# Kernel optimization log

Measured on AMD Instinct MI355X. Metric: run time of the kernel, lower is better.

Reference implementation:

```python
import jax, jax.numpy as jnp
import numpy as np

N = 4096          # total ensemble boxes per frame
M = 20            # MAX_MERGE_NUMS
H = 16            # MergeNet hidden_c
COND_THRES = 0.2
IOU_THRES = 0.3


def setup_inputs() -> dict:
    key = jax.random.key(0)
    ks = jax.random.split(key, 6)
    u = jax.random.uniform(ks[0], (N, 9), dtype=jnp.float32)
    # realistic lidar boxes: centers in a ~140x80x8m range, dims in [0.5, 4.5), heading in [-pi, pi)
    centers = (u[:, 0:3] - 0.5) * jnp.array([140.0, 80.0, 8.0], jnp.float32)
    dims = u[:, 3:6] * 4.0 + 0.5
    heading = (u[:, 6:7] - 0.5) * (2.0 * np.pi)
    extra = u[:, 7:9]  # extra box attrs (cols 7:9), untouched by merge
    pred_boxes = jnp.concatenate([centers, dims, heading, extra], axis=-1)
    pred_scores = jax.random.uniform(ks[1], (N,), dtype=jnp.float32)
    pred_labels = jax.random.randint(ks[2], (N,), 0, 3)
    w1 = (jax.random.normal(ks[3], (M, H), jnp.float32) / np.sqrt(M)).astype(jnp.float32)
    b1 = jnp.zeros((H,), jnp.float32)
    w2 = (jax.random.normal(ks[4], (H, H), jnp.float32) / np.sqrt(H)).astype(jnp.float32)
    b2 = jnp.zeros((H,), jnp.float32)
    w3 = (jax.random.normal(ks[5], (H, 1), jnp.float32) / np.sqrt(H)).astype(jnp.float32)
    b3 = jnp.zeros((1,), jnp.float32)
    return dict(pred_boxes=pred_boxes, pred_scores=pred_scores, pred_labels=pred_labels,
                w1=w1, b1=b1, w2=w2, b2=b2, w3=w3, b3=b3)


def _bev_aligned(b):
    # boxes3d_lidar_to_aligned_bev_boxes: swap dx/dy when |limit_period(heading)| >= pi/4
    ang = b[..., 6] - jnp.floor(b[..., 6] / np.pi + 0.5) * np.pi
    swap = jnp.abs(ang) >= (np.pi / 4)
    dx = jnp.where(swap, b[..., 4], b[..., 3])
    dy = jnp.where(swap, b[..., 3], b[..., 4])
    return jnp.stack([b[..., 0] - dx / 2, b[..., 1] - dy / 2,
                      b[..., 0] + dx / 2, b[..., 1] + dy / 2], axis=-1)


def _iou_one_many(a, b):
    # axis-aligned BEV IoU of one box a[4] vs many b[N,4]
    xmin = jnp.maximum(a[0], b[:, 0]); ymin = jnp.maximum(a[1], b[:, 1])
    xmax = jnp.minimum(a[2], b[:, 2]); ymax = jnp.minimum(a[3], b[:, 3])
    inter = jnp.maximum(xmax - xmin, 0.0) * jnp.maximum(ymax - ymin, 0.0)
    area_a = (a[2] - a[0]) * (a[3] - a[1])
    area_b = (b[:, 2] - b[:, 0]) * (b[:, 3] - b[:, 1])
    return inter / jnp.maximum(area_a + area_b - inter, 1e-6)


def _nms_merge(pred_boxes, pred_scores, pred_labels, w1, b1, w2, b2, w3, b3):
    valid = pred_scores > COND_THRES
    sort_key = jnp.where(valid, pred_scores, -jnp.inf)
    order = jnp.argsort(-sort_key)                 # descending by score; invalid sink
    boxes9 = pred_boxes[order]
    labels = pred_labels[order]
    scores = pred_scores[order]
    suppressed0 = ~valid[order]
    boxes7 = boxes9[:, :7]
    bev0 = _bev_aligned(boxes7)                    # merged boxes get suppressed, so bev is static

    def mergenet(ob):                              # ob: [M, 7] -> merged box [7]
        x = ob.T                                   # [7, M] (k is the feature axis)
        h = jax.nn.relu(x @ w1 + b1)
        h = jax.nn.relu(h @ w2 + b2)
        return (h @ w3 + b3)[:, 0]

    def step(suppressed, i):
        active = ~suppressed[i]
        same = (labels == labels[i]) & (~suppressed)
        iou = _iou_one_many(bev0[i], bev0)         # [N]
        over = (iou > IOU_THRES) & same            # includes self (iou=1)
        count = jnp.sum(over)
        rank = jnp.cumsum(over) - 1                # slot of each overlap, in score order
        tgt = jnp.where(over & (rank < M), rank, M)
        ob = jnp.zeros((M, 7), boxes7.dtype).at[tgt].set(boxes7, mode='drop')
        bi = boxes7[i]
        new_box = jnp.where(count > 1, mergenet(ob), bi)
        new_box = new_box.at[3:6].set(jnp.maximum(new_box[3:6], 1e-5))
        out_box = jnp.where(active, new_box, bi)
        return suppressed | (over & active), (out_box, active)

    _, (merged7, keep) = jax.lax.scan(step, suppressed0, jnp.arange(N))
    out_boxes = jnp.concatenate([merged7, boxes9[:, 7:9]], axis=-1)   # [N, 9]
    return out_boxes, scores, labels, keep


def reference(pred_boxes, pred_scores, pred_labels, w1, b1, w2, b2, w3, b3):
    # Returns fixed-shape (boxes9, scores, labels, keep_mask); rows with keep=False
    # correspond to boxes that torch's dynamic version would have removed.
    return _nms_merge(pred_boxes, pred_scores, pred_labels, w1, b1, w2, b2, w3, b3)
```

## Files before the change

### kernel.cpp

```cpp
#include <hip/hip_runtime.h>
#include <cstdint>

typedef unsigned long long u64;
typedef unsigned int u32;

#define NB 4096
#define NW 64
#define MM 20
#define HH 16
#define COND_THRES 0.2f
#define IOU_THRES 0.3f
#define PI_F  3.14159265358979323846f
#define PI4_F 0.78539816339744830962f

#define NTILE 2080

#define WS_MASK    32768
#define WS_BOX9S   (WS_MASK + NB*NW*8)
#define WS_BEVS    (WS_BOX9S + NB*9*4)
#define WS_SCORES  (WS_BEVS + NB*16)
#define WS_LABELS  (WS_SCORES + NB*4)
#define WS_NBRW    (WS_LABELS + NB*4)
#define WS_SUPSTEP (WS_NBRW + NB*8)
#define WS_CNT     (WS_SUPSTEP + NB*4)
#define WS_SLOTW   (WS_CNT + NB*4)
#define WS_SLOTI   (WS_SLOTW + NB*16)
#define WS_CSARR   (WS_SLOTI + NB*8)

__device__ __forceinline__ u64 sort_key(float s, int i) {
  u32 sb = (s > COND_THRES) ? __float_as_uint(s) : 0u;
  return ((u64)(sb ^ 0xFFFFFFFFu) << 12) | (u64)i;
}

__global__ void __launch_bounds__(256) k_prep(const float* __restrict__ scores,
                                              const float* __restrict__ boxes9,
                                              const int* __restrict__ labels,
                                              float* __restrict__ box9s, float4* __restrict__ bevs,
                                              float* __restrict__ scoress, int* __restrict__ labelss,
                                              u64* __restrict__ nbrw, u32* __restrict__ cnt) {
  #pragma clang fp contract(off)
  __shared__ u64 keys[NB];
  __shared__ u32 part[16][16];
  int tid = threadIdx.x;
  for (int k = tid; k < NB; k += 256) keys[k] = sort_key(scores[k], k);
  __syncthreads();
  int bl = tid & 15;
  int ch = tid >> 4;
  u64 ki = keys[blockIdx.x * 16 + bl];
  int c = 0;
  #pragma unroll 16
  for (int t = 0; t < 256; ++t) c += (keys[(ch << 8) + t] < ki) ? 1 : 0;
  part[bl][ch] = (u32)c;
  __syncthreads();
  if (tid < 16) {
    int i = blockIdx.x * 16 + tid;
    int r = 0;
    #pragma unroll
    for (int q = 0; q < 16; ++q) r += (int)part[tid][q];
    nbrw[i] = 0;
    cnt[i] = 0;
    float b[9];
    #pragma unroll
    for (int f = 0; f < 9; ++f) b[f] = boxes9[i * 9 + f];
    #pragma unroll
    for (int f = 0; f < 9; ++f) box9s[r * 9 + f] = b[f];
    float ang = b[6] - floorf(b[6] / PI_F + 0.5f) * PI_F;
    bool sw = fabsf(ang) >= PI4_F;
    float dx = sw ? b[4] : b[3];
    float dy = sw ? b[3] : b[4];
    bevs[r] = make_float4(b[0] - dx * 0.5f, b[1] - dy * 0.5f,
                          b[0] + dx * 0.5f, b[1] + dy * 0.5f);
    scoress[r] = scores[i];
    labelss[r] = labels[i];
  }
}

__global__ void __launch_bounds__(64) k_mask(const float4* __restrict__ bevs,
                                             const int* __restrict__ labelss,
                                             const float* __restrict__ scoress,
                                             u64* __restrict__ mask,
                                             u64* __restrict__ nbrw,
                                             u32* __restrict__ cnt,
                                             u64* __restrict__ slotW,
                                             u32* __restrict__ slotI,
                                             u64* __restrict__ csArr) {
  #pragma clang fp contract(off)
  __shared__ float4 bj[64];
  __shared__ int lj[64];
  __shared__ u64 tw[64];
  int t = threadIdx.x;
  int b = blockIdx.x;
  int it = (int)((sqrtf(8.0f * (float)b + 1.0f) - 1.0f) * 0.5f);
  while ((it + 1) * (it + 2) / 2 <= b) ++it;
  while (it * (it + 1) / 2 > b) --it;
  int jt = b - it * (it + 1) / 2;
  int j = jt * 64 + t;
  bj[t] = bevs[j];
  lj[t] = labelss[j];
  u64 vj = __ballot(scoress[j] > COND_THRES);
  int i = it * 64 + t;
  float4 a = bevs[i];
  int la = labelss[i];
  float area_a = (a.z - a.x) * (a.w - a.y);
  __syncthreads();
  u64 w = 0;
  #pragma unroll 8
  for (int kk = 0; kk < 64; ++kk) {
    float4 bb = bj[kk];
    float xmin = fmaxf(a.x, bb.x), ymin = fmaxf(a.y, bb.y);
    float xmax = fminf(a.z, bb.z), ymax = fminf(a.w, bb.w);
    float inter = fmaxf(xmax - xmin, 0.0f) * fmaxf(ymax - ymin, 0.0f);
    float area_b = (bb.z - bb.x) * (bb.w - bb.y);
    float iou = inter / fmaxf(area_a + area_b - inter, 1e-6f);
    if ((iou > IOU_THRES) && (la == lj[kk])) w |= (1ull << kk);
  }
  mask[(u64)i * NW + jt] = w;
  if (jt == it) {
    csArr[i] = w & ((1ull << t) - 1ull);
  } else {
    if (w & vj) {
      u32 pos = atomicAdd(&cnt[i], 1u);
      if (pos < 2u) { slotW[i * 2 + pos] = w; slotI[i * 2 + pos] = (u32)jt; }
      atomicOr(&nbrw[i], 1ull << jt);
    }
  }
  if (jt < it) {
    tw[t] = w;
    __syncthreads();
    u64 wT = 0;
    #pragma unroll 8
    for (int k = 0; k < 64; ++k) wT |= ((tw[k] >> t) & 1ull) << k;
    mask[(u64)j * NW + it] = wT;
  }
}

__global__ void __launch_bounds__(1024) k_nms(const u64* __restrict__ mask,
                                              const u64* __restrict__ nbrw,
                                              const u32* __restrict__ cnt,
                                              const u64* __restrict__ slotW,
                                              const u32* __restrict__ slotI,
                                              const u64* __restrict__ csArr,
                                              const float* __restrict__ scoress,
                                              int* __restrict__ supstep) {
  __shared__ u64 csL[NB];
  __shared__ u64 c0L[NB];
  __shared__ u64 c1L[NB];
  __shared__ u64 remL[NB];
  __shared__ u32 i01L[NB];
  __shared__ u64 vwL[64];
  __shared__ u64 keptL[64];
  int tid = threadIdx.x;
  int lane = tid & 63;
  int waveId = tid >> 6;
  #pragma unroll
  for (int s4 = 0; s4 < 4; ++s4) {
    int i = tid + (s4 << 10);
    bool v = scoress[i] > COND_THRES;
    u64 vb = __ballot(v);
    if (lane == 0) vwL[waveId + (s4 << 4)] = vb;
  }
  #pragma unroll
  for (int s4 = 0; s4 < 4; ++s4) {
    int i = tid + (s4 << 10);
    u32 c = cnt[i];
    u64 c0 = 0, c1 = 0; u32 i0 = 0, i1 = 0;
    if (c >= 1u) { c0 = slotW[i * 2];     i0 = slotI[i * 2]; }
    if (c >= 2u) { c1 = slotW[i * 2 + 1]; i1 = slotI[i * 2 + 1]; }
    u32 n = c > 2u ? 2u : c;
    u32 ovf = c > 2u ? 1u : 0u;
    u64 rem = 0;
    if (ovf) rem = nbrw[i] & ~(1ull << i0) & ~(1ull << i1);
    csL[i] = csArr[i];
    c0L[i] = c0; c1L[i] = c1; remL[i] = rem;
    i01L[i] = i0 | (i1 << 6) | (n << 12) | (ovf << 14);
  }
  __syncthreads();
  if (tid < 64) {
    u64 keptW = 0;
    u64 cs_c = csL[lane], c0_c = c0L[lane], c1_c = c1L[lane], rem_c = remL[lane];
    u32 m_c = i01L[lane];
    u64 vws_c = vwL[0];
    for (int s = 0; s < 64; ++s) {
      u64 cs_n = 0, c0_n = 0, c1_n = 0, rem_n = 0, vws_n = 0; u32 m_n = 0;
      if (s < 63) {
        int ip = ((s + 1) << 6) | lane;
        cs_n = csL[ip]; c0_n = c0L[ip]; c1_n = c1L[ip];
        rem_n = remL[ip]; m_n = i01L[ip]; vws_n = vwL[s + 1];
      }
      int w0 = (int)(m_c & 63u), w1 = (int)((m_c >> 6) & 63u);
      u64 k0 = __shfl(keptW, w0);
      u64 k1 = __shfl(keptW, w1);
      bool hk = ((c0_c & k0) | (c1_c & k1)) != 0ull;
      u64 rem = rem_c;
      while (__ballot(rem != 0ull) != 0ull) {
        int w = rem ? __builtin_ctzll(rem) : 0;
        u64 kws = __shfl(keptW, w);
        if (rem) {
          u64 m = mask[(u64)((s << 6) | lane) * NW + w];
          hk = hk || ((m & kws) != 0ull);
          rem &= rem - 1;
        }
      }
      u64 dw = ~vws_c;
      u64 kw = 0;
      bool und = (vws_c >> lane) & 1ull;
      while (true) {
        bool dec = und && ((cs_c & ~dw) == 0ull);
        bool keep = dec && !hk && ((cs_c & kw) == 0ull);
        dw |= __ballot(dec);
        kw |= __ballot(keep);
        und = und && !dec;
        if (__ballot(und) == 0ull) break;
      }
      if (lane == s) keptW = kw;
      cs_c = cs_n; c0_c = c0_n; c1_c = c1_n; rem_c = rem_n; m_c = m_n; vws_c = vws_n;
    }
    keptL[lane] = keptW;
  }
  __syncthreads();
  #pragma unroll
  for (int s4 = 0; s4 < 4; ++s4) {
    int j = tid + (s4 << 10);
    int wj = j >> 6;
    bool valid = (vwL[wj] >> (j & 63)) & 1ull;
    int res;
    if (!valid) {
      res = -1;
    } else {
      res = j;
      u32 m = i01L[j];
      u64 cs = csL[j];
      int cand = 0x7FFFFFFF;
      if (!(m & (1u << 14))) {
        u32 n = (m >> 12) & 3;
        if (n >= 1) {
          int w0 = (int)(m & 63u);
          u64 h = c0L[j] & keptL[w0];
          if (h) { int r = (w0 << 6) + __builtin_ctzll(h); if (r < cand) cand = r; }
        }
        if (n >= 2) {
          int w1 = (int)((m >> 6) & 63u);
          u64 h = c1L[j] & keptL[w1];
          if (h) { int r = (w1 << 6) + __builtin_ctzll(h); if (r < cand) cand = r; }
        }
        { u64 h = cs & keptL[wj];
          if (h) { int r = (wj << 6) + __builtin_ctzll(h); if (r < cand) cand = r; } }
      } else {
        u64 t = nbrw[j];
        while (t) {
          int w = __builtin_ctzll(t);
          t &= t - 1;
          u64 h = mask[(u64)j * NW + w] & keptL[w];
          if (h) { cand = (w << 6) + __builtin_ctzll(h); break; }
        }
        if (cand == 0x7FFFFFFF) {
          u64 h = cs & keptL[wj];
          if (h) cand = (wj << 6) + __builtin_ctzll(h);
        }
      }
      if (cand != 0x7FFFFFFF) res = cand;
    }
    supstep[j] = res;
  }
}

__global__ void __launch_bounds__(64) k_merge(
    const u64* __restrict__ mask, const int* __restrict__ supstep,
    const float* __restrict__ box9s, const float* __restrict__ scoress,
    const int* __restrict__ labelss,
    const float* __restrict__ w1, const float* __restrict__ b1,
    const float* __restrict__ w2, const float* __restrict__ b2,
    const float* __restrict__ w3, const float* __restrict__ b3,
    float* __restrict__ out) {
  #pragma clang fp contract(off)
  __shared__ int candList[MM];
  __shared__ float ob[MM][7];
  __shared__ float h1[7][HH];
  __shared__ float h2[7][HH];
  __shared__ float res[7];
  int i = blockIdx.x;
  int t = threadIdx.x;
  bool active = (supstep[i] == i);
  u64 wq = 0;
  int cnt = 0;
  if (active) {
    u64 w = mask[(u64)i * NW + t];
    while (w) {
      int b = __builtin_ctzll(w);
      w &= w - 1;
      int j = (t << 6) | b;
      if (supstep[j] >= i) { wq |= (1ull << b); cnt++; }
    }
  }
  int incl = cnt;
  #pragma unroll
  for (int off = 1; off < 64; off <<= 1) {
    int v = __shfl_up(incl, off);
    if (t >= off) incl += v;
  }
  int excl = incl - cnt;
  int count = __shfl(incl, 63);
  bool merged = active && (count > 1);
  if (merged && wq) {
    int pos = excl;
    u64 ww = wq;
    while (ww && pos < MM) {
      int b = __builtin_ctzll(ww);
      ww &= ww - 1;
      candList[pos++] = (t << 6) | b;
    }
  }
  __syncthreads();
  if (merged) {
    int nc = count < MM ? count : MM;
    if (t < MM) {
      if (t < nc) {
        int j = candList[t];
        #pragma unroll
        for (int f = 0; f < 7; ++f) ob[t][f] = box9s[j * 9 + f];
      } else {
        #pragma unroll
        for (int f = 0; f < 7; ++f) ob[t][f] = 0.0f;
      }
    }
    __syncthreads();
    for (int o = t; o < 7 * HH; o += 64) {
      int f = o >> 4, hh = o & 15;
      float acc = b1[hh];
      #pragma unroll
      for (int m = 0; m < MM; ++m) acc += ob[m][f] * w1[m * HH + hh];
      h1[f][hh] = fmaxf(acc, 0.0f);
    }
    __syncthreads();
    for (int o = t; o < 7 * HH; o += 64) {
      int f = o >> 4, oo = o & 15;
      float acc = b2[oo];
      #pragma unroll
      for (int k = 0; k < HH; ++k) acc += h1[f][k] * w2[k * HH + oo];
      h2[f][oo] = fmaxf(acc, 0.0f);
    }
    __syncthreads();
    if (t < 7) {
      float acc = b3[0];
      #pragma unroll
      for (int k = 0; k < HH; ++k) acc += h2[t][k] * w3[k];
      if (t >= 3 && t < 6) acc = fmaxf(acc, 1e-5f);
      res[t] = acc;
    }
    __syncthreads();
  }
  if (t < 9) {
    float v = box9s[i * 9 + t];
    if (merged && t < 7) v = res[t];
    out[i * 9 + t] = v;
  }
  if (t == 0) {
    out[NB * 9 + i]          = scoress[i];
    out[NB * 9 + NB + i]     = (float)labelss[i];
    out[NB * 9 + 2 * NB + i] = active ? 1.0f : 0.0f;
  }
}

extern "C" void kernel_launch(void* const* d_in, const int* in_sizes, int n_in,
                              void* d_out, int out_size, void* d_ws, size_t ws_size,
                              hipStream_t stream) {
  const float* boxes9 = (const float*)d_in[0];
  const float* scores = (const float*)d_in[1];
  const int*   labels = (const int*)d_in[2];
  const float* w1 = (const float*)d_in[3];
  const float* b1 = (const float*)d_in[4];
  const float* w2 = (const float*)d_in[5];
  const float* b2 = (const float*)d_in[6];
  const float* w3 = (const float*)d_in[7];
  const float* b3 = (const float*)d_in[8];
  char* ws = (char*)d_ws;
  u64*    mask    = (u64*)(ws + WS_MASK);
  float*  box9s   = (float*)(ws + WS_BOX9S);
  float4* bevs    = (float4*)(ws + WS_BEVS);
  float*  scoress = (float*)(ws + WS_SCORES);
  int*    labelss = (int*)(ws + WS_LABELS);
  u64*    nbrw    = (u64*)(ws + WS_NBRW);
  int*    supstep = (int*)(ws + WS_SUPSTEP);
  u32*    cnt     = (u32*)(ws + WS_CNT);
  u64*    slotW   = (u64*)(ws + WS_SLOTW);
  u32*    slotI   = (u32*)(ws + WS_SLOTI);
  u64*    csArr   = (u64*)(ws + WS_CSARR);
  float*  out     = (float*)d_out;

  hipLaunchKernelGGL(k_prep,  dim3(256),   dim3(256),  0, stream,
                     scores, boxes9, labels, box9s, bevs, scoress, labelss, nbrw, cnt);
  hipLaunchKernelGGL(k_mask,  dim3(NTILE), dim3(64),   0, stream,
                     bevs, labelss, scoress, mask, nbrw, cnt, slotW, slotI, csArr);
  hipLaunchKernelGGL(k_nms,   dim3(1),     dim3(1024), 0, stream,
                     mask, nbrw, cnt, slotW, slotI, csArr, scoress, supstep);
  hipLaunchKernelGGL(k_merge, dim3(NB),    dim3(64),   0, stream,
                     mask, supstep, box9s, scoress, labelss,
                     w1, b1, w2, b2, w3, b3, out);
}
```

Baseline: 125.4 us.

## Prefetch overflow mask words into a shared-memory pool for serial NMS scan

```diff
diff --git a/kernel.cpp b/kernel.cpp
--- a/kernel.cpp
+++ b/kernel.cpp
@@ -14,6 +14,7 @@
 #define PI4_F 0.78539816339744830962f
 
 #define NTILE 2080
+#define POOLP 3072
 
 #define WS_MASK    32768
 #define WS_BOX9S   (WS_MASK + NB*NW*8)
@@ -145,13 +146,17 @@
   __shared__ u64 csL[NB];
   __shared__ u64 c0L[NB];
   __shared__ u64 c1L[NB];
-  __shared__ u64 remL[NB];
-  __shared__ u32 i01L[NB];
+  __shared__ unsigned short i01L[NB];
+  __shared__ u32 povL[NB];
+  __shared__ u64 poolW[POOLP];
+  __shared__ unsigned char poolIdx[POOLP];
   __shared__ u64 vwL[64];
   __shared__ u64 keptL[64];
+  __shared__ u32 poolCnt;
   int tid = threadIdx.x;
   int lane = tid & 63;
   int waveId = tid >> 6;
+  if (tid == 0) poolCnt = 0;
   #pragma unroll
   for (int s4 = 0; s4 < 4; ++s4) {
     int i = tid + (s4 << 10);
@@ -159,6 +164,7 @@
     u64 vb = __ballot(v);
     if (lane == 0) vwL[waveId + (s4 << 4)] = vb;
   }
+  __syncthreads();
   #pragma unroll
   for (int s4 = 0; s4 < 4; ++s4) {
     int i = tid + (s4 << 10);
@@ -168,37 +174,62 @@
     if (c >= 2u) { c1 = slotW[i * 2 + 1]; i1 = slotI[i * 2 + 1]; }
     u32 n = c > 2u ? 2u : c;
     u32 ovf = c > 2u ? 1u : 0u;
-    u64 rem = 0;
-    if (ovf) rem = nbrw[i] & ~(1ull << i0) & ~(1ull << i1);
+    u32 pov = 0;
+    if (ovf) {
+      u64 t = nbrw[i] & ~(1ull << i0) & ~(1ull << i1);
+      u32 len = (u32)__popcll(t);
+      u32 off = atomicAdd(&poolCnt, len);
+      if (off + len <= (u32)POOLP) {
+        u32 k = 0;
+        while (t) {
+          int w = __builtin_ctzll(t);
+          t &= t - 1;
+          poolW[off + k] = mask[(u64)i * NW + w];
+          poolIdx[off + k] = (unsigned char)w;
+          ++k;
+        }
+        pov = off | (len << 16);
+      } else {
+        pov = 0x80000000u;
+      }
+    }
     csL[i] = csArr[i];
-    c0L[i] = c0; c1L[i] = c1; remL[i] = rem;
-    i01L[i] = i0 | (i1 << 6) | (n << 12) | (ovf << 14);
+    c0L[i] = c0; c1L[i] = c1;
+    i01L[i] = (unsigned short)(i0 | (i1 << 6) | (n << 12) | (ovf << 14));
+    povL[i] = pov;
   }
   __syncthreads();
   if (tid < 64) {
     u64 keptW = 0;
-    u64 cs_c = csL[lane], c0_c = c0L[lane], c1_c = c1L[lane], rem_c = remL[lane];
-    u32 m_c = i01L[lane];
+    u64 cs_c = csL[lane], c0_c = c0L[lane], c1_c = c1L[lane];
+    u32 m_c = i01L[lane], p_c = povL[lane];
     u64 vws_c = vwL[0];
     for (int s = 0; s < 64; ++s) {
-      u64 cs_n = 0, c0_n = 0, c1_n = 0, rem_n = 0, vws_n = 0; u32 m_n = 0;
+      u64 cs_n = 0, c0_n = 0, c1_n = 0, vws_n = 0; u32 m_n = 0, p_n = 0;
       if (s < 63) {
         int ip = ((s + 1) << 6) | lane;
         cs_n = csL[ip]; c0_n = c0L[ip]; c1_n = c1L[ip];
-        rem_n = remL[ip]; m_n = i01L[ip]; vws_n = vwL[s + 1];
+        m_n = i01L[ip]; p_n = povL[ip]; vws_n = vwL[s + 1];
       }
       int w0 = (int)(m_c & 63u), w1 = (int)((m_c >> 6) & 63u);
       u64 k0 = __shfl(keptW, w0);
       u64 k1 = __shfl(keptW, w1);
       bool hk = ((c0_c & k0) | (c1_c & k1)) != 0ull;
-      u64 rem = rem_c;
-      while (__ballot(rem != 0ull) != 0ull) {
-        int w = rem ? __builtin_ctzll(rem) : 0;
-        u64 kws = __shfl(keptW, w);
-        if (rem) {
-          u64 m = mask[(u64)((s << 6) | lane) * NW + w];
-          hk = hk || ((m & kws) != 0ull);
-          rem &= rem - 1;
+      if (m_c & (1u << 14)) {
+        if (!(p_c & 0x80000000u)) {
+          u32 off = p_c & 0xFFFFu, len = (p_c >> 16) & 0xFFu;
+          for (u32 k = 0; k < len; ++k) {
+            int w = poolIdx[off + k];
+            hk = hk || ((poolW[off + k] & keptL[w]) != 0ull);
+          }
+        } else {
+          int i = (s << 6) | lane;
+          u64 t = nbrw[i];
+          while (t) {
+            int w = __builtin_ctzll(t);
+            t &= t - 1;
+            hk = hk || ((mask[(u64)i * NW + w] & keptL[w]) != 0ull);
+          }
         }
       }
       u64 dw = ~vws_c;
@@ -213,9 +244,9 @@
         if (__ballot(und) == 0ull) break;
       }
       if (lane == s) keptW = kw;
-      cs_c = cs_n; c0_c = c0_n; c1_c = c1_n; rem_c = rem_n; m_c = m_n; vws_c = vws_n;
-    }
-    keptL[lane] = keptW;
+      if (lane == 0) keptL[s] = kw;
+      cs_c = cs_n; c0_c = c0_n; c1_c = c1_n; m_c = m_n; p_c = p_n; vws_c = vws_n;
+    }
   }
   __syncthreads();
   #pragma unroll
@@ -229,35 +260,39 @@
     } else {
       res = j;
       u32 m = i01L[j];
-      u64 cs = csL[j];
       int cand = 0x7FFFFFFF;
-      if (!(m & (1u << 14))) {
-        u32 n = (m >> 12) & 3;
-        if (n >= 1) {
-          int w0 = (int)(m & 63u);
-          u64 h = c0L[j] & keptL[w0];
-          if (h) { int r = (w0 << 6) + __builtin_ctzll(h); if (r < cand) cand = r; }
+      u32 n = (m >> 12) & 3;
+      if (n >= 1) {
+        int w0 = (int)(m & 63u);
+        u64 h = c0L[j] & keptL[w0];
+        if (h) { int r = (w0 << 6) + __builtin_ctzll(h); if (r < cand) cand = r; }
+      }
+      if (n >= 2) {
+        int w1 = (int)((m >> 6) & 63u);
+        u64 h = c1L[j] & keptL[w1];
+        if (h) { int r = (w1 << 6) + __builtin_ctzll(h); if (r < cand) cand = r; }
+      }
+      if (m & (1u << 14)) {
+        u32 p = povL[j];
+        if (!(p & 0x80000000u)) {
+          u32 off = p & 0xFFFFu, len = (p >> 16) & 0xFFu;
+          for (u32 k = 0; k < len; ++k) {
+            int w = poolIdx[off + k];
+            u64 h = poolW[off + k] & keptL[w];
+            if (h) { int r = (w << 6) + __builtin_ctzll(h); if (r < cand) cand = r; break; }
+          }
+        } else {
+          u64 t = nbrw[j];
+          while (t) {
+            int w = __builtin_ctzll(t);
+            t &= t - 1;
+            u64 h = mask[(u64)j * NW + w] & keptL[w];
+            if (h) { int r = (w << 6) + __builtin_ctzll(h); if (r < cand) cand = r; break; }
+          }
         }
-        if (n >= 2) {
-          int w1 = (int)((m >> 6) & 63u);
-          u64 h = c1L[j] & keptL[w1];
-          if (h) { int r = (w1 << 6) + __builtin_ctzll(h); if (r < cand) cand = r; }
-        }
-        { u64 h = cs & keptL[wj];
-          if (h) { int r = (wj << 6) + __builtin_ctzll(h); if (r < cand) cand = r; } }
-      } else {
-        u64 t = nbrw[j];
-        while (t) {
-          int w = __builtin_ctzll(t);
-          t &= t - 1;
-          u64 h = mask[(u64)j * NW + w] & keptL[w];
-          if (h) { cand = (w << 6) + __builtin_ctzll(h); break; }
-        }
-        if (cand == 0x7FFFFFFF) {
-          u64 h = cs & keptL[wj];
-          if (h) cand = (wj << 6) + __builtin_ctzll(h);
-        }
-      }
+      }
+      { u64 h = csL[j] & keptL[wj];
+        if (h) { int r = (wj << 6) + __builtin_ctzll(h); if (r < cand) cand = r; } }
       if (cand != 0x7FFFFFFF) res = cand;
     }
     supstep[j] = res;
```

After: 123.8 us. Within noise of the previous version (-1.3%).
